# Performance work log

Hardware: AMD Instinct MI355X
Metric: run time of the kernel (lower is better)

The kernel has to match this reference:

```python
import jax, jax.numpy as jnp
import numpy as np

H = 128
M = 50000
L = 400000
EPS = 1e-9


def setup_inputs() -> dict:
    key = jax.random.key(0)
    ks = jax.random.split(key, 24)
    d = {
        'x_emb': jax.random.normal(ks[0], (M, H), jnp.float32),
        'child_h': jax.random.normal(ks[1], (M, H), jnp.float32),
        'child_c': jax.random.normal(ks[2], (M, H), jnp.float32),
        'pair_cand_idx': jax.random.randint(ks[3], (L,), 0, M, jnp.int32),
        'pair_child_idx': jax.random.randint(ks[4], (L,), 0, M, jnp.int32),
    }
    s = 1.0 / np.sqrt(H)
    names = ['Wi_w', 'Ui_w', 'Wf_w', 'Uf_w', 'Wo_w', 'Uo_w', 'Wc_w', 'Uc_w', 'Wa_w', 'Ua_w']
    for i, n in enumerate(names):
        d[n] = jax.random.uniform(ks[5 + i], (H, H), jnp.float32, -s, s)
    for i, n in enumerate(['Wi_b', 'Wf_b', 'Wo_b', 'Wc_b', 'Wa_b']):
        d[n] = jax.random.uniform(ks[15 + i], (H,), jnp.float32, -s, s)
    d['v_w'] = jax.random.uniform(ks[20], (H,), jnp.float32, -s, s)
    return d


def reference(x_emb, child_h, child_c, pair_cand_idx, pair_child_idx,
              Wi_w, Ui_w, Wf_w, Uf_w, Wo_w, Uo_w, Wc_w, Uc_w, Wa_w, Ua_w,
              Wi_b, Wf_b, Wo_b, Wc_b, Wa_b, v_w):
    m = x_emb.shape[0]
    ci, chi = pair_cand_idx, pair_child_idx

    # --- segment attention (torch version runs under no_grad) ---
    Ah = child_h @ Wa_w.T + Wa_b          # [M,H]
    Bx = x_emb @ Ua_w.T                   # [M,H]
    e = jnp.tanh(Ah[chi] + Bx[ci]) @ v_w  # [L]
    seg_max = jax.ops.segment_max(e, ci, num_segments=m)
    x_exp = jnp.exp(e - seg_max[ci])
    seg_sum = jax.ops.segment_sum(x_exp, ci, num_segments=m) + EPS
    attn = x_exp / seg_sum[ci]            # [L]
    h_hat = jax.ops.segment_sum(attn[:, None] * child_h[chi], ci, num_segments=m)  # [M,H]

    # --- tree-LSTM gates ---
    i_j = jax.nn.sigmoid(x_emb @ Wi_w.T + Wi_b + h_hat @ Ui_w.T)
    Wfx = x_emb @ Wf_w.T + Wf_b
    Ufh = child_h @ Uf_w.T
    f_pair = jax.nn.sigmoid(Wfx[ci] + Ufh[chi])                       # [L,H]
    sum_f_c = jax.ops.segment_sum(f_pair * child_c[chi], ci, num_segments=m)
    c_t = jnp.tanh(x_emb @ Wc_w.T + Wc_b + h_hat @ Uc_w.T)
    c = i_j * c_t + sum_f_c
    o_j = jax.nn.sigmoid(x_emb @ Wo_w.T + Wo_b + h_hat @ Uo_w.T)
    h = o_j * jnp.tanh(c)
    return (h, c)
```

## Files before the change

kernel.cpp:

```cpp
#include <hip/hip_runtime.h>
#include <cstdint>
#include <cstddef>

#define H 128
#define PSTRIDE 384

typedef __bf16 v8bf __attribute__((ext_vector_type(8)));
typedef __bf16 v4bf __attribute__((ext_vector_type(4)));
typedef float  v4f  __attribute__((ext_vector_type(4)));

__device__ __forceinline__ float ftanh(float x) {
    return 1.f - 2.f / (1.f + __expf(2.f * x));
}
__device__ __forceinline__ float fsigm(float x) {
    return 1.f / (1.f + __expf(-x));
}

struct MatDesc {
    const __bf16* A;
    int           lda;
    const __bf16* Wb;
    const float*  bias;
    __bf16*       C;
    int           ldc;
};
struct MatBatch { MatDesc m[7]; };
struct WPtrs { const float* w[10]; };

__global__ __launch_bounds__(256) void wconv(WPtrs wp, __bf16* __restrict__ Wb) {
    int i = blockIdx.x * 256 + threadIdx.x;
    if (i >= 10 * 4096) return;
    int mat = i >> 12;
    int off = (i & 4095) << 2;
    v4f a = *(const v4f*)(wp.w[mat] + off);
    v4bf b;
#pragma unroll
    for (int k = 0; k < 4; ++k) b[k] = (__bf16)a[k];
    *(v4bf*)(Wb + mat * 16384 + off) = b;
}

__global__ __launch_bounds__(256) void convert_k(const float* __restrict__ x,
                                                 const float* __restrict__ chh,
                                                 const float* __restrict__ chc,
                                                 __bf16* __restrict__ xe,
                                                 __bf16* __restrict__ P,
                                                 int MH4, int* __restrict__ counts, int M) {
    int i = blockIdx.x * 256 + threadIdx.x;
    if (i < MH4) {
        v4f a = ((const v4f*)x)[i];
        v4f b = ((const v4f*)chh)[i];
        v4f c = ((const v4f*)chc)[i];
        v4bf ab, bb, cb;
#pragma unroll
        for (int k = 0; k < 4; ++k) {
            ab[k] = (__bf16)a[k]; bb[k] = (__bf16)b[k]; cb[k] = (__bf16)c[k];
        }
        ((v4bf*)xe)[i] = ab;
        int m = i >> 5;
        int q = (i & 31) << 2;
        __bf16* prow = P + (size_t)m * PSTRIDE + q;
        *(v4bf*)prow = bb;
        *(v4bf*)(prow + H) = cb;
    }
    if (i < M) counts[i] = 0;
}

__global__ __launch_bounds__(256) void gemm_batch(MatBatch batch, int M) {
    const MatDesc d = batch.m[blockIdx.y];
    __shared__ __bf16 wlds[H][H + 8];

    for (int t = threadIdx.x; t < 2048; t += 256) {
        int n = t >> 4;
        int k = (t & 15) << 3;
        *(v8bf*)&wlds[n][k] = *(const v8bf*)(d.Wb + n * H + k);
    }
    __syncthreads();

    const int wave = threadIdx.x >> 6;
    const int lane = threadIdx.x & 63;
    const int quad = lane >> 4;
    const int l16  = lane & 15;
    const int r0   = blockIdx.x * 64 + wave * 16;

    v4f acc[8];
#pragma unroll
    for (int nt = 0; nt < 8; ++nt) acc[nt] = (v4f){0.f, 0.f, 0.f, 0.f};

    const __bf16* arow = d.A + (size_t)(r0 + l16) * d.lda + quad * 8;
#pragma unroll
    for (int k0 = 0; k0 < H; k0 += 32) {
        v8bf a = *(const v8bf*)(arow + k0);
#pragma unroll
        for (int nt = 0; nt < 8; ++nt) {
            v8bf b = *(const v8bf*)(&wlds[nt * 16 + l16][k0 + quad * 8]);
            acc[nt] = __builtin_amdgcn_mfma_f32_16x16x32_bf16(a, b, acc[nt], 0, 0, 0);
        }
    }

#pragma unroll
    for (int nt = 0; nt < 8; ++nt) {
        int n = nt * 16 + l16;
        float bia = d.bias ? d.bias[n] : 0.f;
#pragma unroll
        for (int r = 0; r < 4; ++r) {
            int m = r0 + quad * 4 + r;
            if (m < M) d.C[(size_t)m * d.ldc + n] = (__bf16)(acc[nt][r] + bia);
        }
    }
}

__global__ __launch_bounds__(256) void edge_e(const __bf16* __restrict__ Ah,
                                              const __bf16* __restrict__ Bx,
                                              const int* __restrict__ ci,
                                              const int* __restrict__ chi,
                                              const float* __restrict__ vw,
                                              float* __restrict__ expe,
                                              int* __restrict__ counts, int L) {
    int tid = threadIdx.x;
    int sub = tid & 15;
    int l = blockIdx.x * 16 + (tid >> 4);
    if (l >= L) return;
    int c = ci[l], ch = chi[l];
    v8bf a = *(const v8bf*)(Ah + (size_t)ch * H + sub * 8);
    v8bf b = *(const v8bf*)(Bx + (size_t)c * H + sub * 8);
    v4f v0 = *(const v4f*)(vw + sub * 8);
    v4f v1 = *(const v4f*)(vw + sub * 8 + 4);
    float s = 0.f;
#pragma unroll
    for (int k = 0; k < 8; ++k) {
        float x = (float)a[k] + (float)b[k];
        float vv = (k < 4) ? v0[k] : v1[k - 4];
        s += ftanh(x) * vv;
    }
    s += __shfl_xor(s, 1);
    s += __shfl_xor(s, 2);
    s += __shfl_xor(s, 4);
    s += __shfl_xor(s, 8);
    if (sub == 0) {
        expe[l] = __expf(s);
        atomicAdd(&counts[c], 1);
    }
}

__global__ __launch_bounds__(1024) void scan_local(const int* __restrict__ counts,
                                                   int* __restrict__ excl,
                                                   int* __restrict__ bsums, int M) {
    __shared__ int s[1024];
    int tid = threadIdx.x;
    int idx = blockIdx.x * 1024 + tid;
    int v = (idx < M) ? counts[idx] : 0;
    s[tid] = v;
    __syncthreads();
    for (int off = 1; off < 1024; off <<= 1) {
        int t = (tid >= off) ? s[tid - off] : 0;
        __syncthreads();
        s[tid] += t;
        __syncthreads();
    }
    if (idx < M) excl[idx] = s[tid] - v;
    if (tid == 1023) bsums[blockIdx.x] = s[1023];
}

__global__ __launch_bounds__(1024) void scan_tops(const int* __restrict__ bsums,
                                                  int* __restrict__ boffs, int nb) {
    __shared__ int s[1024];
    int tid = threadIdx.x;
    int v = (tid < nb) ? bsums[tid] : 0;
    s[tid] = v;
    __syncthreads();
    for (int off = 1; off < 1024; off <<= 1) {
        int t = (tid >= off) ? s[tid - off] : 0;
        __syncthreads();
        s[tid] += t;
        __syncthreads();
    }
    if (tid < nb) boffs[tid] = s[tid] - v;
}

__global__ __launch_bounds__(1024) void scan_add(int* __restrict__ rowptr,
                                                 int* __restrict__ cursor,
                                                 const int* __restrict__ boffs,
                                                 const int* __restrict__ counts, int M) {
    int idx = blockIdx.x * 1024 + threadIdx.x;
    if (idx < M) {
        int v = rowptr[idx] + boffs[blockIdx.x];
        rowptr[idx] = v;
        cursor[idx] = v;
        if (idx == M - 1) rowptr[M] = v + counts[M - 1];
    }
}

__global__ __launch_bounds__(256) void scatter_k(const int* __restrict__ ci,
                                                 int* __restrict__ cursor,
                                                 int* __restrict__ edge_list, int L) {
    int l = blockIdx.x * 256 + threadIdx.x;
    if (l < L) {
        int pos = atomicAdd(&cursor[ci[l]], 1);
        edge_list[pos] = l;
    }
}

__global__ __launch_bounds__(128) void segment_k(const int* __restrict__ rowptr,
                                                 const int* __restrict__ edge_list,
                                                 const int* __restrict__ chi,
                                                 const float* __restrict__ expe,
                                                 const __bf16* __restrict__ Wfx,
                                                 const __bf16* __restrict__ P,
                                                 __bf16* __restrict__ hhat,
                                                 float* __restrict__ sumfc, int M) {
    int g    = threadIdx.x >> 5;
    int lane = threadIdx.x & 31;
    int m = blockIdx.x * 4 + g;
    if (m >= M) return;
    int start = rowptr[m], deg = rowptr[m + 1] - start;

    float part = 0.f;
    for (int j = lane; j < deg; j += 32) part += expe[edge_list[start + j]];
    part += __shfl_xor(part, 1);
    part += __shfl_xor(part, 2);
    part += __shfl_xor(part, 4);
    part += __shfl_xor(part, 8);
    part += __shfl_xor(part, 16);
    float inv = 1.f / (part + 1e-9f);

    int h = lane << 2;
    v4bf wf4 = *(const v4bf*)(Wfx + (size_t)m * H + h);
    float wfx[4];
#pragma unroll
    for (int k = 0; k < 4; ++k) wfx[k] = (float)wf4[k];

    float acch[4] = {0.f, 0.f, 0.f, 0.f};
    float accf[4] = {0.f, 0.f, 0.f, 0.f};

    int j = 0;
    for (; j + 1 < deg; j += 2) {
        int l0 = edge_list[start + j], l1 = edge_list[start + j + 1];
        int c0 = chi[l0], c1 = chi[l1];
        float a0 = expe[l0] * inv, a1 = expe[l1] * inv;
        const __bf16* p0 = P + c0 * PSTRIDE + h;
        const __bf16* p1 = P + c1 * PSTRIDE + h;
        v4bf h0 = *(const v4bf*)p0;
        v4bf c4_0 = *(const v4bf*)(p0 + H);
        v4bf u0 = *(const v4bf*)(p0 + 2 * H);
        v4bf h1 = *(const v4bf*)p1;
        v4bf c4_1 = *(const v4bf*)(p1 + H);
        v4bf u1 = *(const v4bf*)(p1 + 2 * H);
#pragma unroll
        for (int k = 0; k < 4; ++k) {
            acch[k] += a0 * (float)h0[k] + a1 * (float)h1[k];
            accf[k] += fsigm(wfx[k] + (float)u0[k]) * (float)c4_0[k]
                     + fsigm(wfx[k] + (float)u1[k]) * (float)c4_1[k];
        }
    }
    if (j < deg) {
        int l0 = edge_list[start + j];
        int c0 = chi[l0];
        float a0 = expe[l0] * inv;
        const __bf16* p0 = P + c0 * PSTRIDE + h;
        v4bf h0 = *(const v4bf*)p0;
        v4bf c4_0 = *(const v4bf*)(p0 + H);
        v4bf u0 = *(const v4bf*)(p0 + 2 * H);
#pragma unroll
        for (int k = 0; k < 4; ++k) {
            acch[k] += a0 * (float)h0[k];
            accf[k] += fsigm(wfx[k] + (float)u0[k]) * (float)c4_0[k];
        }
    }

    v4bf hb;
    v4f sf;
#pragma unroll
    for (int k = 0; k < 4; ++k) { hb[k] = (__bf16)acch[k]; sf[k] = accf[k]; }
    *(v4bf*)(hhat + (size_t)m * H + h) = hb;
    *(v4f*)(sumfc + (size_t)m * H + h) = sf;
}

__global__ __launch_bounds__(256) void final_k(const __bf16* __restrict__ Xi, const __bf16* __restrict__ Hi,
                                               const __bf16* __restrict__ Xc, const __bf16* __restrict__ Hc,
                                               const __bf16* __restrict__ Xo, const __bf16* __restrict__ Ho,
                                               const float* __restrict__ sumfc,
                                               float* __restrict__ out, int MH4, int MH) {
    int i = blockIdx.x * 256 + threadIdx.x;
    if (i >= MH4) return;
    v4bf xi = ((const v4bf*)Xi)[i], hi = ((const v4bf*)Hi)[i];
    v4bf xc = ((const v4bf*)Xc)[i], hc = ((const v4bf*)Hc)[i];
    v4bf xo = ((const v4bf*)Xo)[i], ho = ((const v4bf*)Ho)[i];
    v4f sf = ((const v4f*)sumfc)[i];
    v4f hout, cout;
#pragma unroll
    for (int k = 0; k < 4; ++k) {
        float ig = fsigm((float)xi[k] + (float)hi[k]);
        float ct = ftanh((float)xc[k] + (float)hc[k]);
        float og = fsigm((float)xo[k] + (float)ho[k]);
        float c = ig * ct + sf[k];
        cout[k] = c;
        hout[k] = og * ftanh(c);
    }
    ((v4f*)out)[i] = hout;
    ((v4f*)(out + MH))[i] = cout;
}

extern "C" void kernel_launch(void* const* d_in, const int* in_sizes, int n_in,
                              void* d_out, int out_size, void* d_ws, size_t ws_size,
                              hipStream_t stream) {
    const float* x_emb   = (const float*)d_in[0];
    const float* child_h = (const float*)d_in[1];
    const float* child_c = (const float*)d_in[2];
    const int*   ci      = (const int*)d_in[3];
    const int*   chi     = (const int*)d_in[4];
    const float* Wi_b = (const float*)d_in[15];
    const float* Wf_b = (const float*)d_in[16];
    const float* Wo_b = (const float*)d_in[17];
    const float* Wc_b = (const float*)d_in[18];
    const float* Wa_b = (const float*)d_in[19];
    const float* vw   = (const float*)d_in[20];

    const int M    = in_sizes[0] / H;
    const int L    = in_sizes[3];
    const int Mpad = (M + 63) & ~63;
    const int MH   = M * H;

    char* p = (char*)d_ws;
    auto alloc = [&](size_t bytes) {
        char* r = p;
        p += (bytes + 255) & ~(size_t)255;
        return (void*)r;
    };
    size_t bfbytes = (size_t)Mpad * H * sizeof(__bf16);
    __bf16* xe16   = (__bf16*)alloc(bfbytes);
    __bf16* P      = (__bf16*)alloc((size_t)Mpad * PSTRIDE * sizeof(__bf16));
    __bf16* hhat16 = (__bf16*)alloc(bfbytes);
    __bf16* Ah16   = (__bf16*)alloc(bfbytes);
    __bf16* Bx16   = (__bf16*)alloc(bfbytes);
    __bf16* Wfx16  = (__bf16*)alloc(bfbytes);
    __bf16* Xi16   = (__bf16*)alloc(bfbytes);
    __bf16* Xc16   = (__bf16*)alloc(bfbytes);
    __bf16* Xo16   = (__bf16*)alloc(bfbytes);
    __bf16* Wb     = (__bf16*)alloc(10 * 16384 * sizeof(__bf16));
    float* sumfc     = (float*)alloc((size_t)MH * 4);
    float* expe      = (float*)alloc((size_t)L * 4);
    int*   edge_list = (int*)alloc((size_t)L * 4);
    int*   counts    = (int*)alloc((size_t)M * 4);
    int*   rowptr    = (int*)alloc((size_t)(M + 1) * 4);
    int*   cursor    = (int*)alloc((size_t)M * 4);
    int*   bsums     = (int*)alloc(1024 * 4);
    int*   boffs     = (int*)alloc(1024 * 4);
    __bf16* Hi16 = Ah16;
    __bf16* Hc16 = Bx16;
    __bf16* Ho16 = Wfx16;

    WPtrs wp;
    for (int k = 0; k < 10; ++k) wp.w[k] = (const float*)d_in[5 + k];
    wconv<<<(10 * 4096 + 255) / 256, 256, 0, stream>>>(wp, Wb);

    const int MH4 = MH / 4;
    convert_k<<<(MH4 + 255) / 256, 256, 0, stream>>>(x_emb, child_h, child_c, xe16, P, MH4, counts, M);

    const __bf16* Wi = Wb + 0 * 16384;
    const __bf16* Ui = Wb + 1 * 16384;
    const __bf16* Wf = Wb + 2 * 16384;
    const __bf16* Uf = Wb + 3 * 16384;
    const __bf16* Wo = Wb + 4 * 16384;
    const __bf16* Uo = Wb + 5 * 16384;
    const __bf16* Wc = Wb + 6 * 16384;
    const __bf16* Uc = Wb + 7 * 16384;
    const __bf16* Wa = Wb + 8 * 16384;
    const __bf16* Ua = Wb + 9 * 16384;

    MatBatch ba{};
    ba.m[0] = MatDesc{P,    PSTRIDE, Wa, Wa_b,    Ah16,    H};
    ba.m[1] = MatDesc{xe16, H,       Ua, nullptr, Bx16,    H};
    ba.m[2] = MatDesc{xe16, H,       Wf, Wf_b,    Wfx16,   H};
    ba.m[3] = MatDesc{P,    PSTRIDE, Uf, nullptr, P + 2*H, PSTRIDE};
    ba.m[4] = MatDesc{xe16, H,       Wi, Wi_b,    Xi16,    H};
    ba.m[5] = MatDesc{xe16, H,       Wc, Wc_b,    Xc16,    H};
    ba.m[6] = MatDesc{xe16, H,       Wo, Wo_b,    Xo16,    H};
    dim3 gA(Mpad / 64, 7);
    gemm_batch<<<gA, 256, 0, stream>>>(ba, M);

    edge_e<<<(L + 15) / 16, 256, 0, stream>>>(Ah16, Bx16, ci, chi, vw, expe, counts, L);

    int nb = (M + 1023) / 1024;
    scan_local<<<nb, 1024, 0, stream>>>(counts, rowptr, bsums, M);
    scan_tops<<<1, 1024, 0, stream>>>(bsums, boffs, nb);
    scan_add<<<nb, 1024, 0, stream>>>(rowptr, cursor, boffs, counts, M);

    scatter_k<<<(L + 255) / 256, 256, 0, stream>>>(ci, cursor, edge_list, L);
    segment_k<<<(M + 3) / 4, 128, 0, stream>>>(rowptr, edge_list, chi, expe, Wfx16, P,
                                               hhat16, sumfc, M);

    MatBatch bb{};
    bb.m[0] = MatDesc{hhat16, H, Ui, nullptr, Hi16, H};
    bb.m[1] = MatDesc{hhat16, H, Uc, nullptr, Hc16, H};
    bb.m[2] = MatDesc{hhat16, H, Uo, nullptr, Ho16, H};
    dim3 gB(Mpad / 64, 3);
    gemm_batch<<<gB, 256, 0, stream>>>(bb, M);

    final_k<<<(MH4 + 255) / 256, 256, 0, stream>>>(Xi16, Hi16, Xc16, Hc16, Xo16, Ho16, sumfc,
                                                   (float*)d_out, MH4, MH);
}
```

Before: 402.3 us.

## Fuse edge attention into segment kernel, merge prep and scan launches, widen GEMM tiles

Drops the separate per-edge score kernel. The segment kernel now computes attention scores itself from Ah rows, which are stored in a fourth slot of the widened P row, and the scatter writes child indices directly instead of edge ids. Weight conversion, input conversion and in-degree counting merge into one prep launch. The three scan kernels become two, and each GEMM wave now computes 32 rows instead of 16. Together these are meant to cut launch count, remove the expe and edge_list round trips, and improve GEMM reuse of the B fragments. The cost is 33% more P storage, recomputing tanh scores for nodes with degree above 64, and more accumulator registers in the GEMM.

```diff
diff --git a/kernel.cpp b/kernel.cpp
--- a/kernel.cpp
+++ b/kernel.cpp
@@ -3,7 +3,7 @@
 #include <cstddef>
 
 #define H 128
-#define PSTRIDE 384
+#define PSTRIDE 512
 
 typedef __bf16 v8bf __attribute__((ext_vector_type(8)));
 typedef __bf16 v4bf __attribute__((ext_vector_type(4)));
@@ -27,25 +27,27 @@
 struct MatBatch { MatDesc m[7]; };
 struct WPtrs { const float* w[10]; };
 
-__global__ __launch_bounds__(256) void wconv(WPtrs wp, __bf16* __restrict__ Wb) {
-    int i = blockIdx.x * 256 + threadIdx.x;
-    if (i >= 10 * 4096) return;
-    int mat = i >> 12;
-    int off = (i & 4095) << 2;
-    v4f a = *(const v4f*)(wp.w[mat] + off);
-    v4bf b;
-#pragma unroll
-    for (int k = 0; k < 4; ++k) b[k] = (__bf16)a[k];
-    *(v4bf*)(Wb + mat * 16384 + off) = b;
-}
-
-__global__ __launch_bounds__(256) void convert_k(const float* __restrict__ x,
-                                                 const float* __restrict__ chh,
-                                                 const float* __restrict__ chc,
-                                                 __bf16* __restrict__ xe,
-                                                 __bf16* __restrict__ P,
-                                                 int MH4, int* __restrict__ counts, int M) {
-    int i = blockIdx.x * 256 + threadIdx.x;
+__global__ __launch_bounds__(256) void prep_k(WPtrs wp, __bf16* __restrict__ Wb,
+                                              const float* __restrict__ x,
+                                              const float* __restrict__ chh,
+                                              const float* __restrict__ chc,
+                                              __bf16* __restrict__ xe,
+                                              __bf16* __restrict__ P,
+                                              const int* __restrict__ ci,
+                                              int* __restrict__ counts,
+                                              int MH4, int L) {
+    int tid = blockIdx.x * 256 + threadIdx.x;
+    if (tid < 40960) {
+        int mat = tid >> 12;
+        int off = (tid & 4095) << 2;
+        v4f a = *(const v4f*)(wp.w[mat] + off);
+        v4bf b;
+#pragma unroll
+        for (int k = 0; k < 4; ++k) b[k] = (__bf16)a[k];
+        *(v4bf*)(Wb + mat * 16384 + off) = b;
+        return;
+    }
+    int i = tid - 40960;
     if (i < MH4) {
         v4f a = ((const v4f*)x)[i];
         v4f b = ((const v4f*)chh)[i];
@@ -61,8 +63,10 @@
         __bf16* prow = P + (size_t)m * PSTRIDE + q;
         *(v4bf*)prow = bb;
         *(v4bf*)(prow + H) = cb;
-    }
-    if (i < M) counts[i] = 0;
+        return;
+    }
+    int l = i - MH4;
+    if (l < L) atomicAdd(&counts[ci[l]], 1);
 }
 
 __global__ __launch_bounds__(256) void gemm_batch(MatBatch batch, int M) {
@@ -80,20 +84,26 @@
     const int lane = threadIdx.x & 63;
     const int quad = lane >> 4;
     const int l16  = lane & 15;
-    const int r0   = blockIdx.x * 64 + wave * 16;
-
-    v4f acc[8];
-#pragma unroll
-    for (int nt = 0; nt < 8; ++nt) acc[nt] = (v4f){0.f, 0.f, 0.f, 0.f};
-
-    const __bf16* arow = d.A + (size_t)(r0 + l16) * d.lda + quad * 8;
+    const int r0   = blockIdx.x * 128 + wave * 32;
+
+    v4f acc0[8], acc1[8];
+#pragma unroll
+    for (int nt = 0; nt < 8; ++nt) {
+        acc0[nt] = (v4f){0.f, 0.f, 0.f, 0.f};
+        acc1[nt] = (v4f){0.f, 0.f, 0.f, 0.f};
+    }
+
+    const __bf16* ar0 = d.A + (size_t)(r0 + l16) * d.lda + quad * 8;
+    const __bf16* ar1 = d.A + (size_t)(r0 + 16 + l16) * d.lda + quad * 8;
 #pragma unroll
     for (int k0 = 0; k0 < H; k0 += 32) {
-        v8bf a = *(const v8bf*)(arow + k0);
+        v8bf a0 = *(const v8bf*)(ar0 + k0);
+        v8bf a1 = *(const v8bf*)(ar1 + k0);
 #pragma unroll
         for (int nt = 0; nt < 8; ++nt) {
             v8bf b = *(const v8bf*)(&wlds[nt * 16 + l16][k0 + quad * 8]);
-            acc[nt] = __builtin_amdgcn_mfma_f32_16x16x32_bf16(a, b, acc[nt], 0, 0, 0);
+            acc0[nt] = __builtin_amdgcn_mfma_f32_16x16x32_bf16(a0, b, acc0[nt], 0, 0, 0);
+            acc1[nt] = __builtin_amdgcn_mfma_f32_16x16x32_bf16(a1, b, acc1[nt], 0, 0, 0);
         }
     }
 
@@ -103,42 +113,11 @@
         float bia = d.bias ? d.bias[n] : 0.f;
 #pragma unroll
         for (int r = 0; r < 4; ++r) {
-            int m = r0 + quad * 4 + r;
-            if (m < M) d.C[(size_t)m * d.ldc + n] = (__bf16)(acc[nt][r] + bia);
+            int m0 = r0 + quad * 4 + r;
+            int m1 = m0 + 16;
+            if (m0 < M) d.C[(size_t)m0 * d.ldc + n] = (__bf16)(acc0[nt][r] + bia);
+            if (m1 < M) d.C[(size_t)m1 * d.ldc + n] = (__bf16)(acc1[nt][r] + bia);
         }
-    }
-}
-
-__global__ __launch_bounds__(256) void edge_e(const __bf16* __restrict__ Ah,
-                                              const __bf16* __restrict__ Bx,
-                                              const int* __restrict__ ci,
-                                              const int* __restrict__ chi,
-                                              const float* __restrict__ vw,
-                                              float* __restrict__ expe,
-                                              int* __restrict__ counts, int L) {
-    int tid = threadIdx.x;
-    int sub = tid & 15;
-    int l = blockIdx.x * 16 + (tid >> 4);
-    if (l >= L) return;
-    int c = ci[l], ch = chi[l];
-    v8bf a = *(const v8bf*)(Ah + (size_t)ch * H + sub * 8);
-    v8bf b = *(const v8bf*)(Bx + (size_t)c * H + sub * 8);
-    v4f v0 = *(const v4f*)(vw + sub * 8);
-    v4f v1 = *(const v4f*)(vw + sub * 8 + 4);
-    float s = 0.f;
-#pragma unroll
-    for (int k = 0; k < 8; ++k) {
-        float x = (float)a[k] + (float)b[k];
-        float vv = (k < 4) ? v0[k] : v1[k - 4];
-        s += ftanh(x) * vv;
-    }
-    s += __shfl_xor(s, 1);
-    s += __shfl_xor(s, 2);
-    s += __shfl_xor(s, 4);
-    s += __shfl_xor(s, 8);
-    if (sub == 0) {
-        expe[l] = __expf(s);
-        atomicAdd(&counts[c], 1);
     }
 }
 
@@ -161,109 +140,140 @@
     if (tid == 1023) bsums[blockIdx.x] = s[1023];
 }
 
-__global__ __launch_bounds__(1024) void scan_tops(const int* __restrict__ bsums,
-                                                  int* __restrict__ boffs, int nb) {
+__global__ __launch_bounds__(1024) void scan_fused(int* __restrict__ rowptr,
+                                                   int* __restrict__ cursor,
+                                                   const int* __restrict__ bsums,
+                                                   const int* __restrict__ counts,
+                                                   int M, int nb) {
     __shared__ int s[1024];
-    int tid = threadIdx.x;
-    int v = (tid < nb) ? bsums[tid] : 0;
-    s[tid] = v;
+    int t = threadIdx.x, b = blockIdx.x;
+    int v = (t < nb) ? bsums[t] : 0;
+    s[t] = v;
     __syncthreads();
     for (int off = 1; off < 1024; off <<= 1) {
-        int t = (tid >= off) ? s[tid - off] : 0;
+        int tt = (t >= off) ? s[t - off] : 0;
         __syncthreads();
-        s[tid] += t;
+        s[t] += tt;
         __syncthreads();
     }
-    if (tid < nb) boffs[tid] = s[tid] - v;
-}
-
-__global__ __launch_bounds__(1024) void scan_add(int* __restrict__ rowptr,
+    int boff = (b == 0) ? 0 : s[b - 1];
+    int idx = b * 1024 + t;
+    if (idx < M) {
+        int val = rowptr[idx] + boff;
+        rowptr[idx] = val;
+        cursor[idx] = val;
+        if (idx == M - 1) rowptr[M] = val + counts[M - 1];
+    }
+}
+
+__global__ __launch_bounds__(256) void scatter_k(const int* __restrict__ ci,
+                                                 const int* __restrict__ chi,
                                                  int* __restrict__ cursor,
-                                                 const int* __restrict__ boffs,
-                                                 const int* __restrict__ counts, int M) {
-    int idx = blockIdx.x * 1024 + threadIdx.x;
-    if (idx < M) {
-        int v = rowptr[idx] + boffs[blockIdx.x];
-        rowptr[idx] = v;
-        cursor[idx] = v;
-        if (idx == M - 1) rowptr[M] = v + counts[M - 1];
-    }
-}
-
-__global__ __launch_bounds__(256) void scatter_k(const int* __restrict__ ci,
-                                                 int* __restrict__ cursor,
-                                                 int* __restrict__ edge_list, int L) {
+                                                 int* __restrict__ payload, int L) {
     int l = blockIdx.x * 256 + threadIdx.x;
     if (l < L) {
         int pos = atomicAdd(&cursor[ci[l]], 1);
-        edge_list[pos] = l;
-    }
-}
-
-__global__ __launch_bounds__(128) void segment_k(const int* __restrict__ rowptr,
-                                                 const int* __restrict__ edge_list,
-                                                 const int* __restrict__ chi,
-                                                 const float* __restrict__ expe,
-                                                 const __bf16* __restrict__ Wfx,
-                                                 const __bf16* __restrict__ P,
-                                                 __bf16* __restrict__ hhat,
-                                                 float* __restrict__ sumfc, int M) {
-    int g    = threadIdx.x >> 5;
-    int lane = threadIdx.x & 31;
-    int m = blockIdx.x * 4 + g;
+        payload[pos] = chi[l];
+    }
+}
+
+__global__ __launch_bounds__(128) void segment_fused(const int* __restrict__ rowptr,
+                                                     const int* __restrict__ payload,
+                                                     const float* __restrict__ vw,
+                                                     const __bf16* __restrict__ Bx,
+                                                     const __bf16* __restrict__ Wfx,
+                                                     const __bf16* __restrict__ P,
+                                                     __bf16* __restrict__ hhat,
+                                                     float* __restrict__ sumfc, int M) {
+    int wl   = threadIdx.x & 63;
+    int half = wl & 32;
+    int l32  = wl & 31;
+    int m = blockIdx.x * 4 + (threadIdx.x >> 5);
     if (m >= M) return;
     int start = rowptr[m], deg = rowptr[m + 1] - start;
-
-    float part = 0.f;
-    for (int j = lane; j < deg; j += 32) part += expe[edge_list[start + j]];
-    part += __shfl_xor(part, 1);
-    part += __shfl_xor(part, 2);
-    part += __shfl_xor(part, 4);
-    part += __shfl_xor(part, 8);
-    part += __shfl_xor(part, 16);
-    float inv = 1.f / (part + 1e-9f);
-
-    int h = lane << 2;
+    int h = l32 << 2;
+
+    v4bf bx4 = *(const v4bf*)(Bx + (size_t)m * H + h);
     v4bf wf4 = *(const v4bf*)(Wfx + (size_t)m * H + h);
-    float wfx[4];
-#pragma unroll
-    for (int k = 0; k < 4; ++k) wfx[k] = (float)wf4[k];
+    v4f  vv  = *(const v4f*)(vw + h);
+    float bxf[4], wff[4];
+#pragma unroll
+    for (int k = 0; k < 4; ++k) { bxf[k] = (float)bx4[k]; wff[k] = (float)wf4[k]; }
+
+    int pl0 = (l32 < deg) ? payload[start + l32] : 0;
+    int pl1 = (32 + l32 < deg) ? payload[start + 32 + l32] : 0;
+
+    int jcap = deg < 64 ? deg : 64;
+    float e0 = 0.f, e1 = 0.f, denom = 0.f;
+
+    for (int j = 0; j < jcap; ++j) {
+        int cj = __shfl((j & 32) ? pl1 : pl0, half | (j & 31), 64);
+        v4bf a4 = *(const v4bf*)(P + (size_t)cj * PSTRIDE + 3 * H + h);
+        float s = 0.f;
+#pragma unroll
+        for (int k = 0; k < 4; ++k) s += ftanh((float)a4[k] + bxf[k]) * vv[k];
+        s += __shfl_xor(s, 1);
+        s += __shfl_xor(s, 2);
+        s += __shfl_xor(s, 4);
+        s += __shfl_xor(s, 8);
+        s += __shfl_xor(s, 16);
+        float ex = __expf(s);
+        denom += ex;
+        if (l32 == (j & 31)) { if (j & 32) e1 = ex; else e0 = ex; }
+    }
+    for (int j = 64; j < deg; ++j) {
+        int cj = payload[start + j];
+        v4bf a4 = *(const v4bf*)(P + (size_t)cj * PSTRIDE + 3 * H + h);
+        float s = 0.f;
+#pragma unroll
+        for (int k = 0; k < 4; ++k) s += ftanh((float)a4[k] + bxf[k]) * vv[k];
+        s += __shfl_xor(s, 1);
+        s += __shfl_xor(s, 2);
+        s += __shfl_xor(s, 4);
+        s += __shfl_xor(s, 8);
+        s += __shfl_xor(s, 16);
+        denom += __expf(s);
+    }
+    float inv = 1.f / (denom + 1e-9f);
 
     float acch[4] = {0.f, 0.f, 0.f, 0.f};
     float accf[4] = {0.f, 0.f, 0.f, 0.f};
-
-    int j = 0;
-    for (; j + 1 < deg; j += 2) {
-        int l0 = edge_list[start + j], l1 = edge_list[start + j + 1];
-        int c0 = chi[l0], c1 = chi[l1];
-        float a0 = expe[l0] * inv, a1 = expe[l1] * inv;
-        const __bf16* p0 = P + c0 * PSTRIDE + h;
-        const __bf16* p1 = P + c1 * PSTRIDE + h;
-        v4bf h0 = *(const v4bf*)p0;
-        v4bf c4_0 = *(const v4bf*)(p0 + H);
-        v4bf u0 = *(const v4bf*)(p0 + 2 * H);
-        v4bf h1 = *(const v4bf*)p1;
-        v4bf c4_1 = *(const v4bf*)(p1 + H);
-        v4bf u1 = *(const v4bf*)(p1 + 2 * H);
+#pragma unroll 2
+    for (int j = 0; j < jcap; ++j) {
+        int src = half | (j & 31);
+        int   cj = __shfl((j & 32) ? pl1 : pl0, src, 64);
+        float ex = __shfl((j & 32) ? e1 : e0, src, 64);
+        float a = ex * inv;
+        const __bf16* pb = P + (size_t)cj * PSTRIDE + h;
+        v4bf h4 = *(const v4bf*)pb;
+        v4bf c4 = *(const v4bf*)(pb + H);
+        v4bf u4 = *(const v4bf*)(pb + 2 * H);
 #pragma unroll
         for (int k = 0; k < 4; ++k) {
-            acch[k] += a0 * (float)h0[k] + a1 * (float)h1[k];
-            accf[k] += fsigm(wfx[k] + (float)u0[k]) * (float)c4_0[k]
-                     + fsigm(wfx[k] + (float)u1[k]) * (float)c4_1[k];
+            acch[k] += a * (float)h4[k];
+            accf[k] += fsigm(wff[k] + (float)u4[k]) * (float)c4[k];
         }
     }
-    if (j < deg) {
-        int l0 = edge_list[start + j];
-        int c0 = chi[l0];
-        float a0 = expe[l0] * inv;
-        const __bf16* p0 = P + c0 * PSTRIDE + h;
-        v4bf h0 = *(const v4bf*)p0;
-        v4bf c4_0 = *(const v4bf*)(p0 + H);
-        v4bf u0 = *(const v4bf*)(p0 + 2 * H);
+    for (int j = 64; j < deg; ++j) {
+        int cj = payload[start + j];
+        const __bf16* pb = P + (size_t)cj * PSTRIDE + h;
+        v4bf a4 = *(const v4bf*)(pb + 3 * H);
+        float s = 0.f;
+#pragma unroll
+        for (int k = 0; k < 4; ++k) s += ftanh((float)a4[k] + bxf[k]) * vv[k];
+        s += __shfl_xor(s, 1);
+        s += __shfl_xor(s, 2);
+        s += __shfl_xor(s, 4);
+        s += __shfl_xor(s, 8);
+        s += __shfl_xor(s, 16);
+        float a = __expf(s) * inv;
+        v4bf h4 = *(const v4bf*)pb;
+        v4bf c4 = *(const v4bf*)(pb + H);
+        v4bf u4 = *(const v4bf*)(pb + 2 * H);
 #pragma unroll
         for (int k = 0; k < 4; ++k) {
-            acch[k] += a0 * (float)h0[k];
-            accf[k] += fsigm(wfx[k] + (float)u0[k]) * (float)c4_0[k];
+            acch[k] += a * (float)h4[k];
+            accf[k] += fsigm(wff[k] + (float)u4[k]) * (float)c4[k];
         }
     }
 
@@ -317,8 +327,9 @@
 
     const int M    = in_sizes[0] / H;
     const int L    = in_sizes[3];
-    const int Mpad = (M + 63) & ~63;
+    const int Mpad = (M + 127) & ~127;
     const int MH   = M * H;
+    const int MH4  = MH / 4;
 
     char* p = (char*)d_ws;
     auto alloc = [&](size_t bytes) {
@@ -330,31 +341,29 @@
     __bf16* xe16   = (__bf16*)alloc(bfbytes);
     __bf16* P      = (__bf16*)alloc((size_t)Mpad * PSTRIDE * sizeof(__bf16));
     __bf16* hhat16 = (__bf16*)alloc(bfbytes);
-    __bf16* Ah16   = (__bf16*)alloc(bfbytes);
     __bf16* Bx16   = (__bf16*)alloc(bfbytes);
     __bf16* Wfx16  = (__bf16*)alloc(bfbytes);
     __bf16* Xi16   = (__bf16*)alloc(bfbytes);
     __bf16* Xc16   = (__bf16*)alloc(bfbytes);
     __bf16* Xo16   = (__bf16*)alloc(bfbytes);
     __bf16* Wb     = (__bf16*)alloc(10 * 16384 * sizeof(__bf16));
-    float* sumfc     = (float*)alloc((size_t)MH * 4);
-    float* expe      = (float*)alloc((size_t)L * 4);
-    int*   edge_list = (int*)alloc((size_t)L * 4);
-    int*   counts    = (int*)alloc((size_t)M * 4);
-    int*   rowptr    = (int*)alloc((size_t)(M + 1) * 4);
-    int*   cursor    = (int*)alloc((size_t)M * 4);
-    int*   bsums     = (int*)alloc(1024 * 4);
-    int*   boffs     = (int*)alloc(1024 * 4);
-    __bf16* Hi16 = Ah16;
-    __bf16* Hc16 = Bx16;
-    __bf16* Ho16 = Wfx16;
+    float* sumfc   = (float*)alloc((size_t)MH * 4);
+    int*   payload = (int*)alloc((size_t)L * 4);
+    int*   counts  = (int*)alloc((size_t)M * 4);
+    int*   rowptr  = (int*)alloc((size_t)(M + 1) * 4);
+    int*   cursor  = (int*)alloc((size_t)M * 4);
+    int*   bsums   = (int*)alloc(1024 * 4);
+    __bf16* Hi16 = Bx16;
+    __bf16* Hc16 = Wfx16;
+    __bf16* Ho16 = P;
+
+    hipMemsetAsync(counts, 0, (size_t)M * 4, stream);
 
     WPtrs wp;
     for (int k = 0; k < 10; ++k) wp.w[k] = (const float*)d_in[5 + k];
-    wconv<<<(10 * 4096 + 255) / 256, 256, 0, stream>>>(wp, Wb);
-
-    const int MH4 = MH / 4;
-    convert_k<<<(MH4 + 255) / 256, 256, 0, stream>>>(x_emb, child_h, child_c, xe16, P, MH4, counts, M);
+    int prep_items = 40960 + MH4 + L;
+    prep_k<<<(prep_items + 255) / 256, 256, 0, stream>>>(wp, Wb, x_emb, child_h, child_c,
+                                                         xe16, P, ci, counts, MH4, L);
 
     const __bf16* Wi = Wb + 0 * 16384;
     const __bf16* Ui = Wb + 1 * 16384;
@@ -368,32 +377,30 @@
     const __bf16* Ua = Wb + 9 * 16384;
 
     MatBatch ba{};
-    ba.m[0] = MatDesc{P,    PSTRIDE, Wa, Wa_b,    Ah16,    H};
-    ba.m[1] = MatDesc{xe16, H,       Ua, nullptr, Bx16,    H};
-    ba.m[2] = MatDesc{xe16, H,       Wf, Wf_b,    Wfx16,   H};
-    ba.m[3] = MatDesc{P,    PSTRIDE, Uf, nullptr, P + 2*H, PSTRIDE};
-    ba.m[4] = MatDesc{xe16, H,       Wi, Wi_b,    Xi16,    H};
-    ba.m[5] = MatDesc{xe16, H,       Wc, Wc_b,    Xc16,    H};
-    ba.m[6] = MatDesc{xe16, H,       Wo, Wo_b,    Xo16,    H};
-    dim3 gA(Mpad / 64, 7);
+    ba.m[0] = MatDesc{P,    PSTRIDE, Wa, Wa_b,    P + 3 * H, PSTRIDE};
+    ba.m[1] = MatDesc{xe16, H,       Ua, nullptr, Bx16,      H};
+    ba.m[2] = MatDesc{xe16, H,       Wf, Wf_b,    Wfx16,     H};
+    ba.m[3] = MatDesc{P,    PSTRIDE, Uf, nullptr, P + 2 * H, PSTRIDE};
+    ba.m[4] = MatDesc{xe16, H,       Wi, Wi_b,    Xi16,      H};
+    ba.m[5] = MatDesc{xe16, H,       Wc, Wc_b,    Xc16,      H};
+    ba.m[6] = MatDesc{xe16, H,       Wo, Wo_b,    Xo16,      H};
+    dim3 gA(Mpad / 128, 7);
     gemm_batch<<<gA, 256, 0, stream>>>(ba, M);
-
-    edge_e<<<(L + 15) / 16, 256, 0, stream>>>(Ah16, Bx16, ci, chi, vw, expe, counts, L);
 
     int nb = (M + 1023) / 1024;
     scan_local<<<nb, 1024, 0, stream>>>(counts, rowptr, bsums, M);
-    scan_tops<<<1, 1024, 0, stream>>>(bsums, boffs, nb);
-    scan_add<<<nb, 1024, 0, stream>>>(rowptr, cursor, boffs, counts, M);
-
-    scatter_k<<<(L + 255) / 256, 256, 0, stream>>>(ci, cursor, edge_list, L);
-    segment_k<<<(M + 3) / 4, 128, 0, stream>>>(rowptr, edge_list, chi, expe, Wfx16, P,
-                                               hhat16, sumfc, M);
+    scan_fused<<<nb, 1024, 0, stream>>>(rowptr, cursor, bsums, counts, M, nb);
+
+    scatter_k<<<(L + 255) / 256, 256, 0, stream>>>(ci, chi, cursor, payload, L);
+
+    segment_fused<<<(M + 3) / 4, 128, 0, stream>>>(rowptr, payload, vw, Bx16, Wfx16, P,
+                                                   hhat16, sumfc, M);
 
     MatBatch bb{};
     bb.m[0] = MatDesc{hhat16, H, Ui, nullptr, Hi16, H};
     bb.m[1] = MatDesc{hhat16, H, Uc, nullptr, Hc16, H};
     bb.m[2] = MatDesc{hhat16, H, Uo, nullptr, Ho16, H};
-    dim3 gB(Mpad / 64, 3);
+    dim3 gB(Mpad / 128, 3);
     gemm_batch<<<gB, 256, 0, stream>>>(bb, M);
 
     final_k<<<(MH4 + 255) / 256, 256, 0, stream>>>(Xi16, Hi16, Xc16, Hc16, Xo16, Ho16, sumfc,
```

Result: no change. 402.0 us (-0.1%).
